# Optimization experiments

Measured on AMD Instinct MI355X. Metric: run time of the kernel, lower is better.

The kernel has to match this reference:

```python
import jax, jax.numpy as jnp
import numpy as np

N = 50000      # nodes
E = 200000     # edges
F_IN = 128     # input features
H = 1024       # hidden
C = 16         # classes
K = 3          # TAGConv hops
EPS = 1e-5


def setup_inputs() -> dict:
    key = jax.random.key(0)
    ks = jax.random.split(key, 12)
    s = 0.02
    x = jax.random.normal(ks[0], (N, F_IN), jnp.float32)
    edge_index = jax.random.randint(ks[1], (2, E), 0, N, dtype=jnp.int64)
    weight = jax.random.uniform(ks[2], (E,), jnp.float32)
    return {
        "x": x,
        "edge_index": edge_index,
        "weight": weight,
        "W1": jax.random.normal(ks[3], (K + 1, F_IN, H), jnp.float32) * s,
        "b1": jnp.zeros((H,), jnp.float32),
        "g1": jnp.ones((H,), jnp.float32),
        "be1": jnp.zeros((H,), jnp.float32),
        "a1": jnp.ones((H,), jnp.float32),
        "W2": jax.random.normal(ks[4], (K + 1, H, H), jnp.float32) * s,
        "b2": jnp.zeros((H,), jnp.float32),
        "g2": jnp.ones((H,), jnp.float32),
        "be2": jnp.zeros((H,), jnp.float32),
        "a2": jnp.ones((H,), jnp.float32),
        "W3": jax.random.normal(ks[5], (K + 1, H, C), jnp.float32) * s,
        "b3": jnp.zeros((C,), jnp.float32),
    }


def _edge_norm(weight, src, dst):
    # gcn_norm without self-loops: deg from edge weights at target nodes
    deg = jax.ops.segment_sum(weight, dst, num_segments=N)
    safe = jnp.where(deg > 0, deg, 1.0)
    dinv = jnp.where(deg > 0, jax.lax.rsqrt(safe), 0.0)
    norm_w = dinv[src] * weight * dinv[dst]
    cnt = jax.ops.segment_sum(jnp.ones((E,), weight.dtype), dst, num_segments=N)
    cnt_inv = jnp.where(cnt > 0, 1.0 / jnp.where(cnt > 0, cnt, 1.0), 0.0)
    return norm_w, cnt_inv


def _tagconv(x, W, b, src, dst, norm_w, cnt_inv):
    # out = sum_k lin_k(x_k), x_k = mean-aggr of norm_w * x_{k-1}[src] at dst
    out = x @ W[0]
    h = x
    for k in range(1, K + 1):
        msg = norm_w[:, None] * h[src]                       # [E, d]
        h = jax.ops.segment_sum(msg, dst, num_segments=N) * cnt_inv[:, None]
        out = out + h @ W[k]
    return out + b


def _graphnorm(x, g, be, a):
    # single graph: per-graph stats = global stats over nodes
    mean = jnp.mean(x, axis=0)
    out = x - a * mean
    var = jnp.mean(out * out, axis=0)
    return g * out / jnp.sqrt(var + EPS) + be


def reference(x, edge_index, weight, W1, b1, g1, be1, a1,
              W2, b2, g2, be2, a2, W3, b3):
    src, dst = edge_index[0], edge_index[1]
    norm_w, cnt_inv = _edge_norm(weight, src, dst)
    h = jax.nn.elu(_tagconv(x, W1, b1, src, dst, norm_w, cnt_inv))
    h = _graphnorm(h, g1, be1, a1)
    h = jax.nn.elu(_tagconv(h, W2, b2, src, dst, norm_w, cnt_inv))
    h = _graphnorm(h, g2, be2, a2)
    return _tagconv(h, W3, b3, src, dst, norm_w, cnt_inv)
```

## Files before the change

kernel.cpp:

```cpp
#include <hip/hip_runtime.h>
#include <hip/hip_bf16.h>
#include <math.h>

#define N_NODES 50000
#define N_EDGES 200000
#define FIN 128
#define HID 1024
#define NCLS 16
#define EPSN 1e-5f
#define NPAD 50048
#define MT 391
#define EPITCH 136

typedef __attribute__((ext_vector_type(8))) short short8;
typedef __attribute__((ext_vector_type(8))) unsigned short ushort8;
typedef __attribute__((ext_vector_type(4))) unsigned short u16x4;
typedef __attribute__((ext_vector_type(4))) float f32x4;

static __device__ __forceinline__ float bf2f(unsigned short u) {
  union { unsigned int i; float f; } v; v.i = ((unsigned int)u) << 16; return v.f;
}
static __device__ __forceinline__ unsigned short f2bf(float f) {
  __hip_bfloat16 h = __float2bfloat16(f);
  return *(unsigned short*)&h;
}

#define ASYNC16(gsrc, ldst)                                                   \
  __builtin_amdgcn_global_load_lds(                                           \
      (const __attribute__((address_space(1))) void*)(gsrc),                  \
      (__attribute__((address_space(3))) void*)(ldst), 16, 0, 0)


__global__ __launch_bounds__(256) void k_deg_cnt(const int* __restrict__ dst,
                                                 const float* __restrict__ w,
                                                 float* deg, int* cnt) {
  int e = blockIdx.x * 256 + threadIdx.x;
  if (e < N_EDGES) {
    int d = dst[e];
    atomicAdd(&deg[d], w[e]);
    atomicAdd(&cnt[d], 1);
  }
}

__global__ __launch_bounds__(256) void k_normw_cntinv(const int* __restrict__ src,
                                                      const int* __restrict__ dst,
                                                      const float* __restrict__ w,
                                                      const float* __restrict__ deg,
                                                      const int* __restrict__ cnt,
                                                      float* __restrict__ normw,
                                                      float* __restrict__ cnt_inv) {
  int e = blockIdx.x * 256 + threadIdx.x;
  if (e < N_EDGES) {
    float ds = deg[src[e]], dd = deg[dst[e]];
    float a = ds > 0.f ? rsqrtf(ds) : 0.f;
    float b = dd > 0.f ? rsqrtf(dd) : 0.f;
    normw[e] = a * w[e] * b;
  }
  if (e < N_NODES) {
    int c = cnt[e];
    cnt_inv[e] = c > 0 ? 1.f / (float)c : 0.f;
  }
}

__global__ __launch_bounds__(1024) void k_scan_a(const int* __restrict__ cnt,
                                                 int* __restrict__ rowptr,
                                                 int* __restrict__ bsums) {
  __shared__ int sm[1024];
  int tid = threadIdx.x;
  int i = blockIdx.x * 1024 + tid;
  int v = (i < N_NODES) ? cnt[i] : 0;
  sm[tid] = v;
  __syncthreads();
  for (int off = 1; off < 1024; off <<= 1) {
    int t = (tid >= off) ? sm[tid - off] : 0;
    __syncthreads();
    sm[tid] += t;
    __syncthreads();
  }
  if (i < N_NODES) rowptr[i] = sm[tid] - v;
  if (tid == 1023) bsums[blockIdx.x] = sm[1023];
}

__global__ void k_scan_b(int* bsums, int nb) {
  if (threadIdx.x == 0 && blockIdx.x == 0) {
    int s = 0;
    for (int i = 0; i < nb; ++i) { int t = bsums[i]; bsums[i] = s; s += t; }
  }
}

__global__ __launch_bounds__(1024) void k_scan_c(int* __restrict__ rowptr,
                                                 const int* __restrict__ bsums) {
  int i = blockIdx.x * 1024 + threadIdx.x;
  if (i < N_NODES) rowptr[i] += bsums[blockIdx.x];
}

__global__ __launch_bounds__(256) void k_fill(const int* __restrict__ src,
                                              const int* __restrict__ dst,
                                              const float* __restrict__ normw,
                                              const float* __restrict__ cnt_inv,
                                              const int* __restrict__ rowptr,
                                              int* __restrict__ fill,
                                              int2* __restrict__ csr_ew) {
  int e = blockIdx.x * 256 + threadIdx.x;
  if (e < N_EDGES) {
    int d = dst[e];
    int pos = rowptr[d] + atomicAdd(&fill[d], 1);
    csr_ew[pos] = make_int2(src[e], __float_as_int(normw[e] * cnt_inv[d]));
  }
}


__global__ void k_transpose_bf16(const float* __restrict__ in,
                                 __hip_bfloat16* __restrict__ out, int K, int N) {
  __shared__ float tile[32][33];
  int kb = blockIdx.x * 32, nb = blockIdx.y * 32;
  int tx = threadIdx.x, ty = threadIdx.y;
  for (int i = ty; i < 32; i += 8) tile[i][tx] = in[(size_t)(kb + i) * N + nb + tx];
  __syncthreads();
  for (int i = ty; i < 32; i += 8)
    out[(size_t)(nb + i) * K + kb + tx] = __float2bfloat16(tile[tx][i]);
}

__global__ void k_transpose_scale_bf16(const float* __restrict__ in,
                                       __hip_bfloat16* __restrict__ out, int K, int N,
                                       const float* __restrict__ alpha) {
  __shared__ float tile[32][33];
  int kb = blockIdx.x * 32, nb = blockIdx.y * 32;
  int tx = threadIdx.x, ty = threadIdx.y;
  for (int i = ty; i < 32; i += 8) tile[i][tx] = in[(size_t)(kb + i) * N + nb + tx];
  __syncthreads();
  float sc = alpha[(kb + tx) & (HID - 1)];
  for (int i = ty; i < 32; i += 8)
    out[(size_t)(nb + i) * K + kb + tx] = __float2bfloat16(tile[tx][i] * sc);
}

__global__ __launch_bounds__(256) void k_ck_part(const float* __restrict__ W2,
                                                 const float* __restrict__ beta,
                                                 const float* __restrict__ b2,
                                                 float* __restrict__ ck) {
  int k3 = blockIdx.x;
  int ch = blockIdx.y;
  int tid = threadIdx.x;
  float acc[4] = {0.f, 0.f, 0.f, 0.f};
  const float* Wk = W2 + (size_t)k3 * HID * HID;
  int i0 = ch * 64;
  for (int in = i0; in < i0 + 64; ++in) {
    float s = beta[in];
    const float* row = Wk + (size_t)in * HID;
#pragma unroll
    for (int j = 0; j < 4; ++j) acc[j] += s * row[tid + j * 256];
  }
#pragma unroll
  for (int j = 0; j < 4; ++j) {
    float v = acc[j];
    if (k3 == 0 && ch == 0) v += b2[tid + j * 256];
    atomicAdd(&ck[k3 * HID + tid + j * 256], v);
  }
}

__global__ __launch_bounds__(64) void k_ck3(const float* __restrict__ W3,
                                            const float* __restrict__ beta,
                                            float* __restrict__ ck3) {
  int t = threadIdx.x;
  int k = t >> 4, j = t & 15;
  float acc = 0.f;
  for (int in = 0; in < HID; ++in)
    acc += beta[in] * W3[((size_t)k * HID + in) * 16 + j];
  ck3[t] = acc;
}

__global__ __launch_bounds__(256) void k_packw3(const float* __restrict__ W3,
                                                __hip_bfloat16* __restrict__ W3T,
                                                const float* __restrict__ alpha) {
  int idx = blockIdx.x * 256 + threadIdx.x;
  if (idx < 4 * 1024 * 16) {
    int k3 = idx >> 14, r = idx & 16383, k = r >> 4, j = r & 15;
    W3T[(size_t)(k3 * 16 + j) * 1024 + k] = __float2bfloat16(W3[idx] * alpha[k]);
  }
}

__global__ __launch_bounds__(256) void k_x_to_bf16(const float* __restrict__ x,
                                                   unsigned short* __restrict__ xc) {
  int i = blockIdx.x * 256 + threadIdx.x;
  if (i < N_NODES * FIN / 4) {
    int n = i >> 5, c4 = i & 31;
    const float4 v = ((const float4*)x)[i];
    u16x4 o;
    o[0] = f2bf(v.x); o[1] = f2bf(v.y); o[2] = f2bf(v.z); o[3] = f2bf(v.w);
    *(u16x4*)&xc[(size_t)n * 512 + c4 * 4] = o;
  }
}


template <int W>
__global__ __launch_bounds__(256) void k_spmm_v(
    const unsigned short* __restrict__ src_t, int sp,
    unsigned short* __restrict__ dst_t, int dp,
    const int* __restrict__ rowptr, const int* __restrict__ cnt,
    const int2* __restrict__ csr_ew) {
  constexpr int G = W / 8;
  int gl = blockIdx.x * 256 + threadIdx.x;
  int node = gl / G;
  if (node >= N_NODES) return;
  int fl = (gl % G) * 8;
  int beg = rowptr[node], end = beg + cnt[node];
  float acc[8] = {0.f, 0.f, 0.f, 0.f, 0.f, 0.f, 0.f, 0.f};
  int i = beg;
  for (; i + 1 < end; i += 2) {
    int2 e0 = csr_ew[i], e1 = csr_ew[i + 1];
    float w0 = __int_as_float(e0.y), w1 = __int_as_float(e1.y);
    ushort8 v0 = *(const ushort8*)&src_t[(size_t)e0.x * sp + fl];
    ushort8 v1 = *(const ushort8*)&src_t[(size_t)e1.x * sp + fl];
#pragma unroll
    for (int j = 0; j < 8; ++j) acc[j] += w0 * bf2f(v0[j]) + w1 * bf2f(v1[j]);
  }
  if (i < end) {
    int2 e0 = csr_ew[i];
    float w0 = __int_as_float(e0.y);
    ushort8 v0 = *(const ushort8*)&src_t[(size_t)e0.x * sp + fl];
#pragma unroll
    for (int j = 0; j < 8; ++j) acc[j] += w0 * bf2f(v0[j]);
  }
  ushort8 o;
#pragma unroll
  for (int j = 0; j < 8; ++j) o[j] = f2bf(acc[j]);
  *(ushort8*)&dst_t[(size_t)node * dp + fl] = o;
}

__global__ __launch_bounds__(256) void k_spmm16(const float* __restrict__ src_t, int sp,
                                                const float* __restrict__ addend, int ap,
                                                const float* __restrict__ b3,
                                                float* __restrict__ out, int op,
                                                const int* __restrict__ rowptr,
                                                const int* __restrict__ cnt,
                                                const int2* __restrict__ csr_ew) {
  int idx = blockIdx.x * 256 + threadIdx.x;
  if (idx >= N_NODES * 16) return;
  int node = idx >> 4, f = idx & 15;
  int beg = rowptr[node], ne = cnt[node];
  float acc = 0.f;
  for (int i = 0; i < ne; ++i) {
    int2 e = csr_ew[beg + i];
    acc += __int_as_float(e.y) * src_t[(size_t)e.x * sp + f];
  }
  float r = acc + addend[(size_t)node * ap + f];
  if (b3) r += b3[f];
  out[(size_t)node * op + f] = r;
}


template <int STATS>
__global__ __launch_bounds__(256, 4) void k_gemm(
    const unsigned short* __restrict__ A, int lda,
    const unsigned short* __restrict__ BT, int ldb,
    const unsigned short* __restrict__ Cinit, int ldci,
    void* __restrict__ Cout, int ldc, int cbf16,
    int M, int Nout, int K,
    const float* __restrict__ bias, int do_elu,
    float* __restrict__ stats_out, int stats_off) {
  __shared__ __align__(16) unsigned short smem[128 * EPITCH];
  int tid = threadIdx.x;
  int wave = tid >> 6, lane = tid & 63;
  int wm = wave >> 1, wn = wave & 1;
  int l15 = lane & 15, quad = lane >> 4;
  int im = blockIdx.y, in_ = blockIdx.x;

  f32x4 acc[4][4];
  if (Cinit) {
    {
      int r = tid >> 1, hf = tid & 1;
      const unsigned short* gsrc =
          &Cinit[(size_t)(im * 128 + r) * ldci + in_ * 128 + hf * 64];
#pragma unroll
      for (int v = 0; v < 8; ++v)
        *(ushort8*)&smem[r * EPITCH + hf * 64 + v * 8] = *(const ushort8*)&gsrc[v * 8];
    }
    __syncthreads();
#pragma unroll
    for (int i = 0; i < 4; ++i)
#pragma unroll
      for (int j = 0; j < 4; ++j)
#pragma unroll
        for (int reg = 0; reg < 4; ++reg)
          acc[i][j][reg] =
              bf2f(smem[(wm * 64 + i * 16 + quad * 4 + reg) * EPITCH + wn * 64 + j * 16 + l15]);
    __syncthreads();
  } else {
#pragma unroll
    for (int i = 0; i < 4; ++i)
#pragma unroll
      for (int j = 0; j < 4; ++j) acc[i][j] = (f32x4){0.f, 0.f, 0.f, 0.f};
  }

  int srow = tid >> 2;
  int sl = (tid & 3) ^ (srow & 3) ^ ((srow >> 2) & 3);
  const unsigned short* gA0 = &A[(size_t)(im * 128 + srow) * lda + sl * 8];
  const unsigned short* gA1 = &A[(size_t)(im * 128 + 64 + srow) * lda + sl * 8];
  const unsigned short* gB0 = &BT[(size_t)(in_ * 128 + srow) * ldb + sl * 8];
  const unsigned short* gB1 = &BT[(size_t)(in_ * 128 + 64 + srow) * ldb + sl * 8];
  unsigned short* ldsA = smem;
  unsigned short* ldsB = smem + 8192;
  int woff0 = (wave * 64) * 8;
  int woff1 = (256 + wave * 64) * 8;
  int rsl = (quad ^ (l15 & 3) ^ (l15 >> 2)) * 8;

  auto stage = [&](int k0, int p) {
    ASYNC16(gA0 + k0, &ldsA[p * 4096 + woff0]);
    ASYNC16(gA1 + k0, &ldsA[p * 4096 + woff1]);
    ASYNC16(gB0 + k0, &ldsB[p * 4096 + woff0]);
    ASYNC16(gB1 + k0, &ldsB[p * 4096 + woff1]);
  };
  auto compute = [&](int p) {
    short8 af[4], bf[4];
#pragma unroll
    for (int i = 0; i < 4; ++i)
      af[i] = *(const short8*)&ldsA[p * 4096 + (wm * 64 + i * 16 + l15) * 32 + rsl];
#pragma unroll
    for (int j = 0; j < 4; ++j)
      bf[j] = *(const short8*)&ldsB[p * 4096 + (wn * 64 + j * 16 + l15) * 32 + rsl];
#pragma unroll
    for (int i = 0; i < 4; ++i)
#pragma unroll
      for (int j = 0; j < 4; ++j)
        acc[i][j] = __builtin_amdgcn_mfma_f32_16x16x32_bf16(af[i], bf[j], acc[i][j], 0, 0, 0);
  };

  stage(0, 0);
  __syncthreads();
  int p = 0;
  for (int k0 = 32; k0 < K; k0 += 32) {
    stage(k0, p ^ 1);
    compute(p);
    __syncthreads();
    p ^= 1;
  }
  compute(p);
  __syncthreads();

  if (cbf16) {
    float sl0[4], sl2[4];
    if (STATS) {
#pragma unroll
      for (int j = 0; j < 4; ++j) { sl0[j] = 0.f; sl2[j] = 0.f; }
    }
#pragma unroll
    for (int i = 0; i < 4; ++i)
#pragma unroll
      for (int j = 0; j < 4; ++j) {
        int cg = in_ * 128 + wn * 64 + j * 16 + l15;
        float bv = bias ? bias[cg] : 0.f;
#pragma unroll
        for (int reg = 0; reg < 4; ++reg) {
          float v = acc[i][j][reg] + bv;
          if (do_elu) v = v > 0.f ? v : expm1f(v);
          unsigned short b = f2bf(v);
          smem[(wm * 64 + i * 16 + quad * 4 + reg) * EPITCH + wn * 64 + j * 16 + l15] = b;
          if (STATS) {
            int r = im * 128 + wm * 64 + i * 16 + quad * 4 + reg;
            if (r < M) {
              float vq = bf2f(b);
              sl0[j] += vq; sl2[j] += vq * vq;
            }
          }
        }
      }
    __syncthreads();
    {
      int r = tid >> 1, hf = tid & 1;
      unsigned short* gdst =
          (unsigned short*)Cout + (size_t)(im * 128 + r) * ldc + in_ * 128 + hf * 64;
#pragma unroll
      for (int v = 0; v < 8; ++v)
        *(ushort8*)&gdst[v * 8] = *(const ushort8*)&smem[r * EPITCH + hf * 64 + v * 8];
    }
    if (STATS) {
      __syncthreads();
      float* fs = (float*)smem;
      int slot = wm * 4 + quad;
#pragma unroll
      for (int j = 0; j < 4; ++j) {
        int c = wn * 64 + j * 16 + l15;
        fs[slot * 128 + c] = sl0[j];
        fs[1024 + slot * 128 + c] = sl2[j];
      }
      __syncthreads();
      if (tid < 128) {
        float a0 = 0.f, a1 = 0.f;
#pragma unroll
        for (int s = 0; s < 8; ++s) {
          a0 += fs[s * 128 + tid];
          a1 += fs[1024 + s * 128 + tid];
        }
        atomicAdd(&stats_out[stats_off + in_ * 128 + tid], a0);
        atomicAdd(&stats_out[HID + stats_off + in_ * 128 + tid], a1);
      }
    }
  } else {
#pragma unroll
    for (int i = 0; i < 4; ++i) {
      int r0 = im * 128 + wm * 64 + i * 16 + quad * 4;
#pragma unroll
      for (int j = 0; j < 4; ++j) {
        int c = in_ * 128 + wn * 64 + j * 16 + l15;
        if (c < Nout) {
#pragma unroll
          for (int reg = 0; reg < 4; ++reg) {
            int r = r0 + reg;
            if (r < M) {
              float v = acc[i][j][reg];
              if (bias) v += bias[c];
              if (do_elu) v = v > 0.f ? v : expm1f(v);
              ((float*)Cout)[(size_t)r * ldc + c] = v;
            }
          }
        }
      }
    }
  }
}


__global__ __launch_bounds__(256) void k_finalize(const float* __restrict__ g,
                                                  const float* __restrict__ be,
                                                  const float* __restrict__ a,
                                                  float* __restrict__ stats) {
  int f = blockIdx.x * 256 + threadIdx.x;
  if (f < HID) {
    float m = stats[f] / (float)N_NODES;
    float ex2 = stats[HID + f] / (float)N_NODES;
    float av = a[f];
    float var = ex2 - 2.f * av * m * m + av * av * m * m;
    float alpha = g[f] * rsqrtf(var + EPSN);
    stats[2 * HID + f] = alpha;
    stats[3 * HID + f] = be[f] - alpha * av * m;
  }
}


extern "C" void kernel_launch(void* const* d_in, const int* in_sizes, int n_in,
                              void* d_out, int out_size, void* d_ws, size_t ws_size,
                              hipStream_t stream) {
  const float* x   = (const float*)d_in[0];
  const int*   ei  = (const int*)d_in[1];
  const float* w   = (const float*)d_in[2];
  const float* W1  = (const float*)d_in[3];
  const float* b1  = (const float*)d_in[4];
  const float* g1  = (const float*)d_in[5];
  const float* be1 = (const float*)d_in[6];
  const float* a1  = (const float*)d_in[7];
  const float* W2  = (const float*)d_in[8];
  const float* b2  = (const float*)d_in[9];
  const float* g2  = (const float*)d_in[10];
  const float* be2 = (const float*)d_in[11];
  const float* a2  = (const float*)d_in[12];
  const float* W3  = (const float*)d_in[13];
  const float* b3  = (const float*)d_in[14];
  float* out = (float*)d_out;

  const int* srcI = ei;
  const int* dstI = ei + N_EDGES;

  char* base = (char*)d_ws;
  size_t off = 0;
  auto alloc = [&](size_t bytes) -> char* {
    char* p = base + off;
    off += (bytes + 255) & ~(size_t)255;
    return p;
  };

  float* deg      = (float*)alloc(N_NODES * 4);
  int*   cnt      = (int*)alloc(N_NODES * 4);
  float* cnt_inv  = (float*)alloc(N_NODES * 4);
  float* normw    = (float*)alloc(N_EDGES * 4);
  int*   rowptr   = (int*)alloc((N_NODES + 1) * 4);
  int*   fill     = (int*)alloc(N_NODES * 4);
  int*   bsums    = (int*)alloc(64 * 4);
  int2*  csr_ew   = (int2*)alloc((size_t)N_EDGES * 8);
  float* stats    = (float*)alloc(4 * HID * 4);
  float* ck       = (float*)alloc(4 * HID * 4);
  float* ck3      = (float*)alloc(64 * 4);
  __hip_bfloat16* W1T = (__hip_bfloat16*)alloc((size_t)1024 * 512 * 2);
  __hip_bfloat16* W2T = (__hip_bfloat16*)alloc((size_t)1024 * 4096 * 2);
  __hip_bfloat16* W3T = (__hip_bfloat16*)alloc((size_t)128 * 1024 * 2);
  const size_t FT = (size_t)NPAD * HID * 2;
  unsigned short* T0 = (unsigned short*)alloc(FT);
  unsigned short* T1 = (unsigned short*)alloc(FT);
  size_t rem = (ws_size > off) ? (ws_size - off) : 0;
  bool full = rem >= FT + 1024;
  unsigned short *T2 = nullptr, *Q = nullptr, *R = nullptr;
  int wcols = 0;
  if (full) {
    T2 = (unsigned short*)alloc(FT);
  } else {
    wcols = 512;
    if (rem < 2 * (size_t)NPAD * 512 * 2 + 1024) wcols = 256;
    if (wcols == 256 && rem < 2 * (size_t)NPAD * 256 * 2 + 1024) wcols = 128;
    Q = (unsigned short*)alloc((size_t)NPAD * wcols * 2);
    R = (unsigned short*)alloc((size_t)NPAD * wcols * 2);
  }
  float* Z  = (float*)T0;
  float* t0 = (float*)((char*)T0 + (size_t)16 * 1024 * 1024);
  float* t1 = (float*)((char*)T0 + (size_t)24 * 1024 * 1024);
  (void)n_in; (void)in_sizes; (void)out_size;

  const int EB = (N_EDGES + 255) / 256;

  (void)hipMemsetAsync(deg, 0, N_NODES * 4, stream);
  (void)hipMemsetAsync(cnt, 0, N_NODES * 4, stream);
  (void)hipMemsetAsync(fill, 0, N_NODES * 4, stream);
  k_deg_cnt<<<EB, 256, 0, stream>>>(dstI, w, deg, cnt);
  k_normw_cntinv<<<EB, 256, 0, stream>>>(srcI, dstI, w, deg, cnt, normw, cnt_inv);
  k_scan_a<<<49, 1024, 0, stream>>>(cnt, rowptr, bsums);
  k_scan_b<<<1, 64, 0, stream>>>(bsums, 49);
  k_scan_c<<<49, 1024, 0, stream>>>(rowptr, bsums);
  k_fill<<<EB, 256, 0, stream>>>(srcI, dstI, normw, cnt_inv, rowptr, fill, csr_ew);

  k_transpose_bf16<<<dim3(512 / 32, 1024 / 32), dim3(32, 8), 0, stream>>>(W1, W1T, 512, 1024);

  const unsigned short* W2Tu = (const unsigned short*)W2T;

  k_x_to_bf16<<<(N_NODES * FIN / 4 + 255) / 256, 256, 0, stream>>>(x, T1);
  {
    int blocks = (N_NODES * 16 + 255) / 256;
    for (int k = 1; k <= 3; ++k)
      k_spmm_v<128><<<blocks, 256, 0, stream>>>(
          T1 + (k - 1) * FIN, 512, T1 + k * FIN, 512,
          rowptr, cnt, csr_ew);
  }
  (void)hipMemsetAsync(stats, 0, 2 * HID * 4, stream);
  k_gemm<1><<<dim3(8, MT), 256, 0, stream>>>(
      T1, 512, (const unsigned short*)W1T, 512,
      nullptr, 0, T0, HID, 1, N_NODES, HID, 512, b1, 1, stats, 0);
  k_finalize<<<4, 256, 0, stream>>>(g1, be1, a1, stats);
  k_transpose_scale_bf16<<<dim3(4096 / 32, 1024 / 32), dim3(32, 8), 0, stream>>>(
      W2, W2T, 4096, 1024, stats + 2 * HID);
  (void)hipMemsetAsync(ck, 0, 4 * HID * 4, stream);
  k_ck_part<<<dim3(4, 16), 256, 0, stream>>>(W2, stats + 3 * HID, b2, ck);

  if (full) {
    const int SPB = (N_NODES * 128 + 255) / 256;
    k_gemm<0><<<dim3(8, MT), 256, 0, stream>>>(
        T0, 1024, W2Tu + 3 * 1024, 4096,
        nullptr, 0, T1, 1024, 1, N_NODES, 1024, 1024, ck + 3 * 1024, 0, nullptr, 0);
    k_spmm_v<1024><<<SPB, 256, 0, stream>>>(T1, 1024, T2, 1024,
                                            rowptr, cnt, csr_ew);
    k_gemm<0><<<dim3(8, MT), 256, 0, stream>>>(
        T0, 1024, W2Tu + 2 * 1024, 4096,
        T2, 1024, T1, 1024, 1, N_NODES, 1024, 1024, ck + 2 * 1024, 0, nullptr, 0);
    k_spmm_v<1024><<<SPB, 256, 0, stream>>>(T1, 1024, T2, 1024,
                                            rowptr, cnt, csr_ew);
    k_gemm<0><<<dim3(8, MT), 256, 0, stream>>>(
        T0, 1024, W2Tu + 1 * 1024, 4096,
        T2, 1024, T1, 1024, 1, N_NODES, 1024, 1024, ck + 1 * 1024, 0, nullptr, 0);
    k_spmm_v<1024><<<SPB, 256, 0, stream>>>(T1, 1024, T2, 1024,
                                            rowptr, cnt, csr_ew);
    (void)hipMemsetAsync(stats, 0, 2 * HID * 4, stream);
    k_gemm<1><<<dim3(8, MT), 256, 0, stream>>>(
        T0, 1024, W2Tu + 0 * 1024, 4096,
        T2, 1024, T1, 1024, 1, N_NODES, 1024, 1024, ck + 0 * 1024, 1, stats, 0);
  } else {
    auto spmm_w = [&](const unsigned short* s, unsigned short* d) {
      int blocks = (N_NODES * (wcols / 8) + 255) / 256;
      if (wcols == 512)
        k_spmm_v<512><<<blocks, 256, 0, stream>>>(s, wcols, d, wcols,
            rowptr, cnt, csr_ew);
      else if (wcols == 256)
        k_spmm_v<256><<<blocks, 256, 0, stream>>>(s, wcols, d, wcols,
            rowptr, cnt, csr_ew);
      else
        k_spmm_v<128><<<blocks, 256, 0, stream>>>(s, wcols, d, wcols,
            rowptr, cnt, csr_ew);
    };
    (void)hipMemsetAsync(stats, 0, 2 * HID * 4, stream);
    for (int c = 0; c < HID; c += wcols) {
      const unsigned short* Wb = W2Tu + (size_t)c * 4096;
      k_gemm<0><<<dim3(wcols / 128, MT), 256, 0, stream>>>(
          T0, 1024, Wb + 3 * 1024, 4096,
          nullptr, 0, Q, wcols, 1, N_NODES, wcols, 1024, ck + 3 * 1024 + c, 0, nullptr, 0);
      spmm_w(Q, R);
      k_gemm<0><<<dim3(wcols / 128, MT), 256, 0, stream>>>(
          T0, 1024, Wb + 2 * 1024, 4096,
          R, wcols, Q, wcols, 1, N_NODES, wcols, 1024, ck + 2 * 1024 + c, 0, nullptr, 0);
      spmm_w(Q, R);
      k_gemm<0><<<dim3(wcols / 128, MT), 256, 0, stream>>>(
          T0, 1024, Wb + 1 * 1024, 4096,
          R, wcols, Q, wcols, 1, N_NODES, wcols, 1024, ck + 1 * 1024 + c, 0, nullptr, 0);
      spmm_w(Q, R);
      k_gemm<1><<<dim3(wcols / 128, MT), 256, 0, stream>>>(
          T0, 1024, Wb + 0 * 1024, 4096,
          R, wcols, T1 + c, 1024, 1, N_NODES, wcols, 1024, ck + 0 * 1024 + c, 1, stats, c);
    }
  }
  k_finalize<<<4, 256, 0, stream>>>(g2, be2, a2, stats);
  k_packw3<<<(65536 + 255) / 256, 256, 0, stream>>>(W3, W3T, stats + 2 * HID);
  k_ck3<<<1, 64, 0, stream>>>(W3, stats + 3 * HID, ck3);

  k_gemm<0><<<dim3(1, MT), 256, 0, stream>>>(
      T1, 1024, (const unsigned short*)W3T, 1024,
      nullptr, 0, Z, 64, 0, N_NODES, 64, 1024, ck3, 0, nullptr, 0);
  const int SB = (N_NODES * 16 + 255) / 256;
  k_spmm16<<<SB, 256, 0, stream>>>(Z + 48, 64, Z + 32, 64, nullptr, t0, 16,
                                   rowptr, cnt, csr_ew);
  k_spmm16<<<SB, 256, 0, stream>>>(t0, 16, Z + 16, 64, nullptr, t1, 16,
                                   rowptr, cnt, csr_ew);
  k_spmm16<<<SB, 256, 0, stream>>>(t1, 16, Z + 0, 64, b3, out, 16,
                                   rowptr, cnt, csr_ew);
}
```

Before: 1.832 ms.

## Split-K the final classifier GEMM and widen the small bias-reduction kernels

The last GEMM, with 64 output columns, previously ran one block per 128-row tile over the full K=1024. It now splits K into four chunks across blockIdx.x and accumulates into a zeroed Z with atomicAdd. The bias is added only by the first chunk. The k_ck_part and k_ck3 reductions are spread across more blocks: k_ck3 goes from a single 64-thread block to 64 blocks with a shared-memory tree reduction. The aim is more parallelism for under-occupied small kernels, at the cost of an extra memset and atomic traffic on Z.

After: 1.845 ms. Within noise of the previous version (+0.7%).

```diff
diff --git a/kernel.cpp b/kernel.cpp
--- a/kernel.cpp
+++ b/kernel.cpp
@@ -143,8 +143,8 @@
   int tid = threadIdx.x;
   float acc[4] = {0.f, 0.f, 0.f, 0.f};
   const float* Wk = W2 + (size_t)k3 * HID * HID;
-  int i0 = ch * 64;
-  for (int in = i0; in < i0 + 64; ++in) {
+  int i0 = ch * 16;
+  for (int in = i0; in < i0 + 16; ++in) {
     float s = beta[in];
     const float* row = Wk + (size_t)in * HID;
 #pragma unroll
@@ -158,15 +158,23 @@
   }
 }
 
-__global__ __launch_bounds__(64) void k_ck3(const float* __restrict__ W3,
-                                            const float* __restrict__ beta,
-                                            float* __restrict__ ck3) {
-  int t = threadIdx.x;
-  int k = t >> 4, j = t & 15;
+__global__ __launch_bounds__(256) void k_ck3(const float* __restrict__ W3,
+                                             const float* __restrict__ beta,
+                                             float* __restrict__ ck3) {
+  __shared__ float sm[256];
+  int b = blockIdx.x;
+  int k = b >> 4, j = b & 15;
+  int tid = threadIdx.x;
   float acc = 0.f;
-  for (int in = 0; in < HID; ++in)
+  for (int in = tid; in < HID; in += 256)
     acc += beta[in] * W3[((size_t)k * HID + in) * 16 + j];
-  ck3[t] = acc;
+  sm[tid] = acc;
+  __syncthreads();
+  for (int s = 128; s > 0; s >>= 1) {
+    if (tid < s) sm[tid] += sm[tid + s];
+    __syncthreads();
+  }
+  if (tid == 0) ck3[b] = sm[0];
 }
 
 __global__ __launch_bounds__(256) void k_packw3(const float* __restrict__ W3,
@@ -249,7 +257,7 @@
 }
 
 
-template <int STATS>
+template <int STATS, int ATOMIC = 0>
 __global__ __launch_bounds__(256, 4) void k_gemm(
     const unsigned short* __restrict__ A, int lda,
     const unsigned short* __restrict__ BT, int ldb,
@@ -263,7 +271,10 @@
   int wave = tid >> 6, lane = tid & 63;
   int wm = wave >> 1, wn = wave & 1;
   int l15 = lane & 15, quad = lane >> 4;
-  int im = blockIdx.y, in_ = blockIdx.x;
+  int im = blockIdx.y;
+  int in_ = ATOMIC ? 0 : blockIdx.x;
+  int kbeg = ATOMIC ? (int)blockIdx.x * (K >> 2) : 0;
+  int kend = ATOMIC ? kbeg + (K >> 2) : K;
 
   f32x4 acc[4][4];
   if (Cinit) {
@@ -325,10 +336,10 @@
         acc[i][j] = __builtin_amdgcn_mfma_f32_16x16x32_bf16(af[i], bf[j], acc[i][j], 0, 0, 0);
   };
 
-  stage(0, 0);
+  stage(kbeg, 0);
   __syncthreads();
   int p = 0;
-  for (int k0 = 32; k0 < K; k0 += 32) {
+  for (int k0 = kbeg + 32; k0 < kend; k0 += 32) {
     stage(k0, p ^ 1);
     compute(p);
     __syncthreads();
@@ -408,9 +419,12 @@
             int r = r0 + reg;
             if (r < M) {
               float v = acc[i][j][reg];
-              if (bias) v += bias[c];
+              if (bias && (!ATOMIC || blockIdx.x == 0)) v += bias[c];
               if (do_elu) v = v > 0.f ? v : expm1f(v);
-              ((float*)Cout)[(size_t)r * ldc + c] = v;
+              if (ATOMIC)
+                atomicAdd(&((float*)Cout)[(size_t)r * ldc + c], v);
+              else
+                ((float*)Cout)[(size_t)r * ldc + c] = v;
             }
           }
         }
@@ -535,7 +549,7 @@
   k_transpose_scale_bf16<<<dim3(4096 / 32, 1024 / 32), dim3(32, 8), 0, stream>>>(
       W2, W2T, 4096, 1024, stats + 2 * HID);
   (void)hipMemsetAsync(ck, 0, 4 * HID * 4, stream);
-  k_ck_part<<<dim3(4, 16), 256, 0, stream>>>(W2, stats + 3 * HID, b2, ck);
+  k_ck_part<<<dim3(4, 64), 256, 0, stream>>>(W2, stats + 3 * HID, b2, ck);
 
   if (full) {
     const int SPB = (N_NODES * 128 + 255) / 256;
@@ -593,9 +607,10 @@
   }
   k_finalize<<<4, 256, 0, stream>>>(g2, be2, a2, stats);
   k_packw3<<<(65536 + 255) / 256, 256, 0, stream>>>(W3, W3T, stats + 2 * HID);
-  k_ck3<<<1, 64, 0, stream>>>(W3, stats + 3 * HID, ck3);
-
-  k_gemm<0><<<dim3(1, MT), 256, 0, stream>>>(
+  k_ck3<<<64, 256, 0, stream>>>(W3, stats + 3 * HID, ck3);
+
+  (void)hipMemsetAsync(Z, 0, (size_t)N_NODES * 64 * 4, stream);
+  k_gemm<0, 1><<<dim3(4, MT), 256, 0, stream>>>(
       T1, 1024, (const unsigned short*)W3T, 1024,
       nullptr, 0, Z, 64, 0, N_NODES, 64, 1024, ck3, 0, nullptr, 0);
   const int SB = (N_NODES * 16 + 255) / 256;
```
